# Optimization experiments

Hardware: AMD Instinct MI355X
Metric: run time of the kernel (lower is better)

## Reference

```python
import jax, jax.numpy as jnp
import numpy as np

B, N_IN, O, IN_L, OUT_L = 256, 1152, 10, 8, 16
ITERS = 3
EPS = 1e-7

def squash(s, eps):
    # norm over the capsule-length axis (-2), keepdim, as in the torch code
    dot = jnp.sum(s * s, axis=-2, keepdims=True)
    return (dot / (1.0 + dot) / jnp.sqrt(dot + eps)) * s

def setup_inputs() -> dict:
    key = jax.random.key(0)
    k1, k2, k3 = jax.random.split(key, 3)
    x = jax.random.normal(k1, (B, N_IN, IN_L, 1), dtype=jnp.float32)
    weight = 0.05 * jax.random.normal(k2, (1, N_IN, O, IN_L, OUT_L), dtype=jnp.float32)
    bias = 0.05 * jax.random.normal(k3, (1, 1, O, OUT_L, 1), dtype=jnp.float32)
    return {"x": x, "weight": weight, "bias": bias}

def reference(x, weight, bias):
    # u_hat[b,n,o,k] = sum_i W[0,n,o,i,k] * x[b,n,i,0]  -> (B, N, O, K, 1)
    u_hat = jnp.einsum('noik,bni->bnok', weight[0], x[..., 0])[..., None]
    u_det = jax.lax.stop_gradient(u_hat)
    b_ij = jnp.zeros((x.shape[0], N_IN, O, 1, 1), dtype=x.dtype)
    v = None
    for r in range(ITERS):
        c = jax.nn.softmax(b_ij, axis=2)          # routing coefficients over out caps
        u = u_hat if r == ITERS - 1 else u_det    # detached except last iter
        s = jnp.sum(c * u, axis=1, keepdims=True) + bias  # (B,1,O,K,1)
        v = squash(s, EPS)
        if r != ITERS - 1:
            # agreement: sum over capsule-length axis 3 -> (B,N,O,1,1)
            b_ij = b_ij + jnp.sum(u_det * v, axis=3, keepdims=True)
    return v
```

## Files before the change

### kernel.cpp

```cpp
#include <hip/hip_runtime.h>
#include <hip/hip_bf16.h>

#define BB   256
#define NIN  1152
#define OO   10
#define IL   8
#define OL   16
#define ROW  (OO*OL)
#define EPSQ 1e-7f
#define NT   4
#define BT   32

typedef unsigned short ushx8 __attribute__((ext_vector_type(8)));

__device__ __forceinline__ float bf2f(unsigned short h) {
    unsigned u = ((unsigned)h) << 16;
    return __builtin_bit_cast(float, u);
}

__global__ __launch_bounds__(160) void caps_build(
    const float* __restrict__ x, const float* __restrict__ w,
    unsigned short* __restrict__ u)
{
    __shared__ float4 wl4[NT][321];
    __shared__ float4 xl4[BT * 8];
    const int t  = threadIdx.x;
    const int n0 = blockIdx.x * NT;
    const int b0 = blockIdx.y * BT;

    const float4* wg = reinterpret_cast<const float4*>(w) + (size_t)n0 * 320;
    #pragma unroll
    for (int jj = 0; jj < 8; ++jj) {
        const int j   = t + jj * 160;
        const int row = j / 320;
        const int lin = j - row * 320;
        const int o   = lin >> 5;
        const int rem = lin & 31;
        const int i   = rem >> 2;
        const int kh  = rem & 3;
        wl4[row][(o << 5) | ((i ^ (o & 1)) << 2) | kh] = wg[j];
    }
    const float4* xg = reinterpret_cast<const float4*>(x);
    {
        int j = t;
        xl4[j] = xg[((size_t)(b0 + (j >> 3)) * NIN + n0) * 2 + (j & 7)];
        j = t + 160;
        if (j < BT * 8)
            xl4[j] = xg[((size_t)(b0 + (j >> 3)) * NIN + n0) * 2 + (j & 7)];
    }
    __syncthreads();

    const int nl = t / 40;
    const int r  = t - nl * 40;
    const int hh = r / 20;
    const int s  = r - hh * 20;
    const int o  = s >> 1;
    const int k8 = s & 1;
    const int p  = o & 1;
    const float4* wbase = &wl4[nl][(o << 5) | (k8 << 1)];
    const float4* xbase = &xl4[(hh * 16) * 8 + nl * 2];
    unsigned short* ub = u + ((size_t)(b0 + hh * 16) * NIN + n0 + nl) * ROW
                           + o * OL + k8 * 8;
    const size_t ustride = (size_t)NIN * ROW;

    for (int bl = 0; bl < 16; bl += 4) {
        float xv[4][IL];
        #pragma unroll
        for (int bb = 0; bb < 4; ++bb) {
            const float4 x0 = xbase[(bl + bb) * 8];
            const float4 x1 = xbase[(bl + bb) * 8 + 1];
            xv[bb][0] = x0.x; xv[bb][1] = x0.y; xv[bb][2] = x0.z; xv[bb][3] = x0.w;
            xv[bb][4] = x1.x; xv[bb][5] = x1.y; xv[bb][6] = x1.z; xv[bb][7] = x1.w;
        }

        float acc[4][8];
        #pragma unroll
        for (int bb = 0; bb < 4; ++bb)
            #pragma unroll
            for (int j = 0; j < 8; ++j) acc[bb][j] = 0.f;

        #pragma unroll
        for (int i = 0; i < IL; ++i) {
            const float4 wlo = wbase[(i ^ p) << 2];
            const float4 whi = wbase[((i ^ p) << 2) | 1];
            const float wv[8] = {wlo.x, wlo.y, wlo.z, wlo.w, whi.x, whi.y, whi.z, whi.w};
            #pragma unroll
            for (int bb = 0; bb < 4; ++bb)
                #pragma unroll
                for (int j = 0; j < 8; ++j)
                    acc[bb][j] = fmaf(wv[j], xv[bb][i], acc[bb][j]);
        }

        #pragma unroll
        for (int bb = 0; bb < 4; ++bb) {
            union { ushx8 v; __hip_bfloat162 h[4]; } pk;
            #pragma unroll
            for (int j = 0; j < 4; ++j)
                pk.h[j] = __float22bfloat162_rn(make_float2(acc[bb][2*j], acc[bb][2*j+1]));
            *reinterpret_cast<ushx8*>(ub + (size_t)(bl + bb) * ustride) = pk.v;
        }
    }
}

__global__ __launch_bounds__(768) void caps_route3(
    const unsigned short* __restrict__ u, const float* __restrict__ bias,
    float* __restrict__ outv)
{
    __shared__ float lds[12][ROW];
    __shared__ float vbuf[ROW];
    const int t  = threadIdx.x;
    const int q  = t & 3;
    const int g  = t >> 2;
    const int wv = t >> 6;
    const int b  = blockIdx.x;
    const unsigned short* ub = u + (size_t)b * NIN * ROW;

    float bsv = 0.f;
    if (t < ROW) bsv = bias[t];
    float vprev = 0.f;

    #pragma unroll
    for (int iter = 0; iter < 3; ++iter) {
        float sp[5][8];
        #pragma unroll
        for (int j = 0; j < 5; ++j)
            #pragma unroll
            for (int e = 0; e < 8; ++e) sp[j][e] = 0.f;

        if (iter == 0) {
            for (int m = 0; m < 6; ++m) {
                const unsigned short* un = ub + (size_t)(g + m * 192) * ROW;
                #pragma unroll
                for (int j = 0; j < 5; ++j) {
                    const ushx8 raw = *reinterpret_cast<const ushx8*>(un + (q + 4 * j) * 8);
                    #pragma unroll
                    for (int e = 0; e < 8; ++e) sp[j][e] += bf2f(raw[e]);
                }
            }
        } else {
            float vs[5][8];
            #pragma unroll
            for (int j = 0; j < 5; ++j) {
                #pragma unroll
                for (int e = 0; e < 8; ++e) vs[j][e] = vbuf[(q + 4 * j) * 8 + e];
            }

            for (int m = 0; m < 6; ++m) {
                const unsigned short* un = ub + (size_t)(g + m * 192) * ROW;
                float uf[5][8];
                #pragma unroll
                for (int j = 0; j < 5; ++j) {
                    const ushx8 raw = *reinterpret_cast<const ushx8*>(un + (q + 4 * j) * 8);
                    #pragma unroll
                    for (int e = 0; e < 8; ++e) uf[j][e] = bf2f(raw[e]);
                }

                float d[5], dd[5];
                #pragma unroll
                for (int j = 0; j < 5; ++j) {
                    float acc = uf[j][0] * vs[j][0];
                    #pragma unroll
                    for (int e = 1; e < 8; ++e) acc = fmaf(uf[j][e], vs[j][e], acc);
                    acc += __shfl_xor(acc, 1, 4);
                    d[j] = acc;
                }
                #pragma unroll
                for (int j = 0; j < 5; ++j) dd[j] = __shfl_xor(d[j], 2, 4);

                float mx = fmaxf(d[0], dd[0]);
                #pragma unroll
                for (int j = 1; j < 5; ++j) mx = fmaxf(mx, fmaxf(d[j], dd[j]));
                float se = 0.f, e_[5];
                #pragma unroll
                for (int j = 0; j < 5; ++j) {
                    e_[j] = __expf(d[j] - mx);
                    se += e_[j] + __expf(dd[j] - mx);
                }
                const float r = 1.f / se;
                #pragma unroll
                for (int j = 0; j < 5; ++j) {
                    const float c = e_[j] * r;
                    #pragma unroll
                    for (int e = 0; e < 8; ++e)
                        sp[j][e] = fmaf(c, uf[j][e], sp[j][e]);
                }
            }
        }

        #pragma unroll
        for (int j = 0; j < 5; ++j)
            #pragma unroll
            for (int e = 0; e < 8; ++e) {
                #pragma unroll
                for (int msk = 4; msk <= 32; msk <<= 1)
                    sp[j][e] += __shfl_xor(sp[j][e], msk);
            }
        if ((t & 63) < 4) {
            #pragma unroll
            for (int j = 0; j < 5; ++j)
                #pragma unroll
                for (int e = 0; e < 8; ++e)
                    lds[wv][(q + 4 * j) * 8 + e] = sp[j][e];
        }
        __syncthreads();

        if (t < ROW) {
            float ssum = 0.f;
            #pragma unroll
            for (int wvi = 0; wvi < 12; ++wvi) ssum += lds[wvi][t];
            const float sv = (iter == 0 ? 0.1f : 1.0f) * ssum + bsv;

            float dq = sv * sv;
            dq += __shfl_xor(dq, 1, 16);
            dq += __shfl_xor(dq, 2, 16);
            dq += __shfl_xor(dq, 4, 16);
            dq += __shfl_xor(dq, 8, 16);
            const float f = dq / ((1.f + dq) * sqrtf(dq + EPSQ));
            const float v = f * sv;

            if (iter == 0) { vbuf[t] = v; vprev = v; }
            else if (iter == 1) { vbuf[t] = v + vprev; }
            else { outv[(size_t)b * ROW + t] = v; }
        }
        __syncthreads();
    }
}

extern "C" void kernel_launch(void* const* d_in, const int* in_sizes, int n_in,
                              void* d_out, int out_size, void* d_ws, size_t ws_size,
                              hipStream_t stream) {
    const float* x    = (const float*)d_in[0];
    const float* w    = (const float*)d_in[1];
    const float* bias = (const float*)d_in[2];
    float* out = (float*)d_out;

    unsigned short* u = (unsigned short*)d_ws;

    caps_build<<<dim3(NIN / NT, BB / BT), 160, 0, stream>>>(x, w, u);
    caps_route3<<<BB, 768, 0, stream>>>(u, bias, out);
}
```

Measured before the change: 78.74 us.

## Split routing into per-iteration passes over two N-halves with finish kernels

Replaces the single fused three-iteration routing kernel (one block per batch) with separate pass kernels per iteration, each launched on a 256x2 grid that splits the input capsules into two halves. Small finish kernels combine the partial sums and apply bias and squash. Per-iteration v vectors go through global workspace instead of LDS. This doubles block count to fill more CUs, at the cost of six extra launches and global round trips between iterations.

```diff
diff --git a/kernel.cpp b/kernel.cpp
--- a/kernel.cpp
+++ b/kernel.cpp
@@ -102,128 +102,134 @@
     }
 }
 
-__global__ __launch_bounds__(768) void caps_route3(
-    const unsigned short* __restrict__ u, const float* __restrict__ bias,
-    float* __restrict__ outv)
+template<int ITER>
+__global__ __launch_bounds__(768) void caps_pass(
+    const unsigned short* __restrict__ u, const float* __restrict__ vin,
+    float* __restrict__ partial)
 {
     __shared__ float lds[12][ROW];
-    __shared__ float vbuf[ROW];
     const int t  = threadIdx.x;
     const int q  = t & 3;
     const int g  = t >> 2;
     const int wv = t >> 6;
     const int b  = blockIdx.x;
-    const unsigned short* ub = u + (size_t)b * NIN * ROW;
-
-    float bsv = 0.f;
-    if (t < ROW) bsv = bias[t];
-    float vprev = 0.f;
-
+    const int sp0 = blockIdx.y;
+    const unsigned short* ub = u + ((size_t)b * NIN + (size_t)sp0 * 576) * ROW;
+
+    float sp[5][8];
     #pragma unroll
-    for (int iter = 0; iter < 3; ++iter) {
-        float sp[5][8];
+    for (int j = 0; j < 5; ++j)
+        #pragma unroll
+        for (int e = 0; e < 8; ++e) sp[j][e] = 0.f;
+
+    if (ITER == 0) {
+        for (int m = 0; m < 3; ++m) {
+            const unsigned short* un = ub + (size_t)(g + m * 192) * ROW;
+            #pragma unroll
+            for (int j = 0; j < 5; ++j) {
+                const ushx8 raw = *reinterpret_cast<const ushx8*>(un + (q + 4 * j) * 8);
+                #pragma unroll
+                for (int e = 0; e < 8; ++e) sp[j][e] += bf2f(raw[e]);
+            }
+        }
+    } else {
+        float vs[5][8];
+        #pragma unroll
+        for (int j = 0; j < 5; ++j) {
+            const float* vp = vin + (size_t)b * ROW + (q + 4 * j) * 8;
+            const float4 a  = *reinterpret_cast<const float4*>(vp);
+            const float4 c4 = *reinterpret_cast<const float4*>(vp + 4);
+            vs[j][0] = a.x;  vs[j][1] = a.y;  vs[j][2] = a.z;  vs[j][3] = a.w;
+            vs[j][4] = c4.x; vs[j][5] = c4.y; vs[j][6] = c4.z; vs[j][7] = c4.w;
+        }
+
+        for (int m = 0; m < 3; ++m) {
+            const unsigned short* un = ub + (size_t)(g + m * 192) * ROW;
+            float uf[5][8];
+            #pragma unroll
+            for (int j = 0; j < 5; ++j) {
+                const ushx8 raw = *reinterpret_cast<const ushx8*>(un + (q + 4 * j) * 8);
+                #pragma unroll
+                for (int e = 0; e < 8; ++e) uf[j][e] = bf2f(raw[e]);
+            }
+
+            float d[5], dd[5];
+            #pragma unroll
+            for (int j = 0; j < 5; ++j) {
+                float acc = uf[j][0] * vs[j][0];
+                #pragma unroll
+                for (int e = 1; e < 8; ++e) acc = fmaf(uf[j][e], vs[j][e], acc);
+                acc += __shfl_xor(acc, 1, 4);
+                d[j] = acc;
+            }
+            #pragma unroll
+            for (int j = 0; j < 5; ++j) dd[j] = __shfl_xor(d[j], 2, 4);
+
+            float mx = fmaxf(d[0], dd[0]);
+            #pragma unroll
+            for (int j = 1; j < 5; ++j) mx = fmaxf(mx, fmaxf(d[j], dd[j]));
+            float se = 0.f, e_[5];
+            #pragma unroll
+            for (int j = 0; j < 5; ++j) {
+                e_[j] = __expf(d[j] - mx);
+                se += e_[j] + __expf(dd[j] - mx);
+            }
+            const float rr = 1.f / se;
+            #pragma unroll
+            for (int j = 0; j < 5; ++j) {
+                const float c = e_[j] * rr;
+                #pragma unroll
+                for (int e = 0; e < 8; ++e)
+                    sp[j][e] = fmaf(c, uf[j][e], sp[j][e]);
+            }
+        }
+    }
+
+    #pragma unroll
+    for (int j = 0; j < 5; ++j)
+        #pragma unroll
+        for (int e = 0; e < 8; ++e) {
+            #pragma unroll
+            for (int msk = 4; msk <= 32; msk <<= 1)
+                sp[j][e] += __shfl_xor(sp[j][e], msk);
+        }
+    if ((t & 63) < 4) {
         #pragma unroll
         for (int j = 0; j < 5; ++j)
             #pragma unroll
-            for (int e = 0; e < 8; ++e) sp[j][e] = 0.f;
-
-        if (iter == 0) {
-            for (int m = 0; m < 6; ++m) {
-                const unsigned short* un = ub + (size_t)(g + m * 192) * ROW;
-                #pragma unroll
-                for (int j = 0; j < 5; ++j) {
-                    const ushx8 raw = *reinterpret_cast<const ushx8*>(un + (q + 4 * j) * 8);
-                    #pragma unroll
-                    for (int e = 0; e < 8; ++e) sp[j][e] += bf2f(raw[e]);
-                }
-            }
-        } else {
-            float vs[5][8];
-            #pragma unroll
-            for (int j = 0; j < 5; ++j) {
-                #pragma unroll
-                for (int e = 0; e < 8; ++e) vs[j][e] = vbuf[(q + 4 * j) * 8 + e];
-            }
-
-            for (int m = 0; m < 6; ++m) {
-                const unsigned short* un = ub + (size_t)(g + m * 192) * ROW;
-                float uf[5][8];
-                #pragma unroll
-                for (int j = 0; j < 5; ++j) {
-                    const ushx8 raw = *reinterpret_cast<const ushx8*>(un + (q + 4 * j) * 8);
-                    #pragma unroll
-                    for (int e = 0; e < 8; ++e) uf[j][e] = bf2f(raw[e]);
-                }
-
-                float d[5], dd[5];
-                #pragma unroll
-                for (int j = 0; j < 5; ++j) {
-                    float acc = uf[j][0] * vs[j][0];
-                    #pragma unroll
-                    for (int e = 1; e < 8; ++e) acc = fmaf(uf[j][e], vs[j][e], acc);
-                    acc += __shfl_xor(acc, 1, 4);
-                    d[j] = acc;
-                }
-                #pragma unroll
-                for (int j = 0; j < 5; ++j) dd[j] = __shfl_xor(d[j], 2, 4);
-
-                float mx = fmaxf(d[0], dd[0]);
-                #pragma unroll
-                for (int j = 1; j < 5; ++j) mx = fmaxf(mx, fmaxf(d[j], dd[j]));
-                float se = 0.f, e_[5];
-                #pragma unroll
-                for (int j = 0; j < 5; ++j) {
-                    e_[j] = __expf(d[j] - mx);
-                    se += e_[j] + __expf(dd[j] - mx);
-                }
-                const float r = 1.f / se;
-                #pragma unroll
-                for (int j = 0; j < 5; ++j) {
-                    const float c = e_[j] * r;
-                    #pragma unroll
-                    for (int e = 0; e < 8; ++e)
-                        sp[j][e] = fmaf(c, uf[j][e], sp[j][e]);
-                }
-            }
-        }
-
-        #pragma unroll
-        for (int j = 0; j < 5; ++j)
-            #pragma unroll
-            for (int e = 0; e < 8; ++e) {
-                #pragma unroll
-                for (int msk = 4; msk <= 32; msk <<= 1)
-                    sp[j][e] += __shfl_xor(sp[j][e], msk);
-            }
-        if ((t & 63) < 4) {
-            #pragma unroll
-            for (int j = 0; j < 5; ++j)
-                #pragma unroll
-                for (int e = 0; e < 8; ++e)
-                    lds[wv][(q + 4 * j) * 8 + e] = sp[j][e];
-        }
-        __syncthreads();
-
-        if (t < ROW) {
-            float ssum = 0.f;
-            #pragma unroll
-            for (int wvi = 0; wvi < 12; ++wvi) ssum += lds[wvi][t];
-            const float sv = (iter == 0 ? 0.1f : 1.0f) * ssum + bsv;
-
-            float dq = sv * sv;
-            dq += __shfl_xor(dq, 1, 16);
-            dq += __shfl_xor(dq, 2, 16);
-            dq += __shfl_xor(dq, 4, 16);
-            dq += __shfl_xor(dq, 8, 16);
-            const float f = dq / ((1.f + dq) * sqrtf(dq + EPSQ));
-            const float v = f * sv;
-
-            if (iter == 0) { vbuf[t] = v; vprev = v; }
-            else if (iter == 1) { vbuf[t] = v + vprev; }
-            else { outv[(size_t)b * ROW + t] = v; }
-        }
-        __syncthreads();
-    }
+            for (int e = 0; e < 8; ++e)
+                lds[wv][(q + 4 * j) * 8 + e] = sp[j][e];
+    }
+    __syncthreads();
+
+    if (t < ROW) {
+        float ssum = 0.f;
+        #pragma unroll
+        for (int wvi = 0; wvi < 12; ++wvi) ssum += lds[wvi][t];
+        partial[((size_t)sp0 * BB + b) * ROW + t] = ssum;
+    }
+}
+
+__global__ __launch_bounds__(192) void caps_finish(
+    const float* __restrict__ partial, const float* __restrict__ bias,
+    const float* __restrict__ prevAdd, float* __restrict__ outv, float scale)
+{
+    const int t = threadIdx.x;
+    if (t >= ROW) return;
+    const int b = blockIdx.x;
+
+    const float s = scale * (partial[(size_t)b * ROW + t]
+                           + partial[((size_t)BB + b) * ROW + t]) + bias[t];
+
+    float d = s * s;
+    d += __shfl_xor(d, 1, 16);
+    d += __shfl_xor(d, 2, 16);
+    d += __shfl_xor(d, 4, 16);
+    d += __shfl_xor(d, 8, 16);
+    const float f = d / ((1.f + d) * sqrtf(d + EPSQ));
+    float v = f * s;
+    if (prevAdd) v += prevAdd[(size_t)b * ROW + t];
+    outv[(size_t)b * ROW + t] = v;
 }
 
 extern "C" void kernel_launch(void* const* d_in, const int* in_sizes, int n_in,
@@ -235,7 +241,17 @@
     float* out = (float*)d_out;
 
     unsigned short* u = (unsigned short*)d_ws;
+    float* partial = (float*)((char*)d_ws + (size_t)BB * NIN * ROW * 2);
+    float* v0  = partial + (size_t)2 * BB * ROW;
+    float* vsb = v0 + (size_t)BB * ROW;
+
+    const dim3 pg(BB, 2);
 
     caps_build<<<dim3(NIN / NT, BB / BT), 160, 0, stream>>>(x, w, u);
-    caps_route3<<<BB, 768, 0, stream>>>(u, bias, out);
-}
+    caps_pass<0><<<pg, 768, 0, stream>>>(u, nullptr, partial);
+    caps_finish<<<BB, 192, 0, stream>>>(partial, bias, nullptr, v0, 0.1f);
+    caps_pass<1><<<pg, 768, 0, stream>>>(u, v0, partial);
+    caps_finish<<<BB, 192, 0, stream>>>(partial, bias, v0, vsb, 1.0f);
+    caps_pass<2><<<pg, 768, 0, stream>>>(u, vsb, partial);
+    caps_finish<<<BB, 192, 0, stream>>>(partial, bias, nullptr, out, 1.0f);
+}
```

Result: slower. 100.3 us (+27.4%).

## Compute first routing iteration directly from x and W, skipping a pass over u

Applied to the files above, without the earlier changes.

The first routing iteration has uniform coefficients, so its weighted sum equals one tenth of the plain sum of u_hat over input capsules. That sum is now computed by a new fp32 GEMM-style kernel that writes per-chunk partial sums, followed by a small squash kernel. The routing kernel then runs only the two remaining iterations, saving one full read of the large bf16 u tensor. In exchange it adds two launches, extra reads of x and W, and a partial-sum buffer in workspace.

```diff
diff --git a/kernel.cpp b/kernel.cpp
--- a/kernel.cpp
+++ b/kernel.cpp
@@ -10,6 +10,7 @@
 #define EPSQ 1e-7f
 #define NT   4
 #define BT   32
+#define GNC  72
 
 typedef unsigned short ushx8 __attribute__((ext_vector_type(8)));
 
@@ -102,9 +103,91 @@
     }
 }
 
-__global__ __launch_bounds__(768) void caps_route3(
+__global__ __launch_bounds__(320) void caps_gemm0(
+    const float* __restrict__ x, const float* __restrict__ w,
+    float* __restrict__ psum)
+{
+    const int t   = threadIdx.x;
+    const int bq  = t / 20;
+    const int oct = t - bq * 20;
+    const int o   = oct >> 1;
+    const int k8  = oct & 1;
+    const int b1  = blockIdx.x * 32 + bq;
+    const int b2  = b1 + 16;
+    const int nc  = blockIdx.y;
+    const int n0  = nc * 16;
+
+    const float* wq  = w + (size_t)n0 * 1280 + o * 128 + k8 * 8;
+    const float* xq1 = x + ((size_t)b1 * NIN + n0) * 8;
+    const float* xq2 = x + ((size_t)b2 * NIN + n0) * 8;
+
+    float a0[8], a1[8];
+    #pragma unroll
+    for (int j = 0; j < 8; ++j) { a0[j] = 0.f; a1[j] = 0.f; }
+
+    for (int nn = 0; nn < 16; ++nn) {
+        const float4 xa0 = *reinterpret_cast<const float4*>(xq1 + nn * 8);
+        const float4 xa1 = *reinterpret_cast<const float4*>(xq1 + nn * 8 + 4);
+        const float4 xb0 = *reinterpret_cast<const float4*>(xq2 + nn * 8);
+        const float4 xb1 = *reinterpret_cast<const float4*>(xq2 + nn * 8 + 4);
+        const float xv0[IL] = {xa0.x, xa0.y, xa0.z, xa0.w, xa1.x, xa1.y, xa1.z, xa1.w};
+        const float xv1[IL] = {xb0.x, xb0.y, xb0.z, xb0.w, xb1.x, xb1.y, xb1.z, xb1.w};
+
+        const float* wn = wq + (size_t)nn * 1280;
+        #pragma unroll
+        for (int i = 0; i < IL; ++i) {
+            const float4 wlo = *reinterpret_cast<const float4*>(wn + i * 16);
+            const float4 whi = *reinterpret_cast<const float4*>(wn + i * 16 + 4);
+            a0[0] = fmaf(wlo.x, xv0[i], a0[0]);  a1[0] = fmaf(wlo.x, xv1[i], a1[0]);
+            a0[1] = fmaf(wlo.y, xv0[i], a0[1]);  a1[1] = fmaf(wlo.y, xv1[i], a1[1]);
+            a0[2] = fmaf(wlo.z, xv0[i], a0[2]);  a1[2] = fmaf(wlo.z, xv1[i], a1[2]);
+            a0[3] = fmaf(wlo.w, xv0[i], a0[3]);  a1[3] = fmaf(wlo.w, xv1[i], a1[3]);
+            a0[4] = fmaf(whi.x, xv0[i], a0[4]);  a1[4] = fmaf(whi.x, xv1[i], a1[4]);
+            a0[5] = fmaf(whi.y, xv0[i], a0[5]);  a1[5] = fmaf(whi.y, xv1[i], a1[5]);
+            a0[6] = fmaf(whi.z, xv0[i], a0[6]);  a1[6] = fmaf(whi.z, xv1[i], a1[6]);
+            a0[7] = fmaf(whi.w, xv0[i], a0[7]);  a1[7] = fmaf(whi.w, xv1[i], a1[7]);
+        }
+    }
+
+    float* p1 = psum + ((size_t)nc * BB + b1) * ROW + oct * 8;
+    float* p2 = psum + ((size_t)nc * BB + b2) * ROW + oct * 8;
+    *reinterpret_cast<float4*>(p1)     = make_float4(a0[0], a0[1], a0[2], a0[3]);
+    *reinterpret_cast<float4*>(p1 + 4) = make_float4(a0[4], a0[5], a0[6], a0[7]);
+    *reinterpret_cast<float4*>(p2)     = make_float4(a1[0], a1[1], a1[2], a1[3]);
+    *reinterpret_cast<float4*>(p2 + 4) = make_float4(a1[4], a1[5], a1[6], a1[7]);
+}
+
+__global__ __launch_bounds__(192) void caps_squash0(
+    const float* __restrict__ psum, const float* __restrict__ bias,
+    float* __restrict__ v0)
+{
+    const int t = threadIdx.x;
+    if (t >= ROW) return;
+    const int b = blockIdx.x;
+
+    float s0 = 0.f, s1 = 0.f, s2 = 0.f, s3 = 0.f;
+    const float* pt = psum + (size_t)b * ROW + t;
+    #pragma unroll
+    for (int ch = 0; ch < GNC; ch += 4) {
+        s0 += pt[(size_t)(ch + 0) * BB * ROW];
+        s1 += pt[(size_t)(ch + 1) * BB * ROW];
+        s2 += pt[(size_t)(ch + 2) * BB * ROW];
+        s3 += pt[(size_t)(ch + 3) * BB * ROW];
+    }
+    const float s = 0.1f * ((s0 + s1) + (s2 + s3)) + bias[t];
+
+    float d = s * s;
+    d += __shfl_xor(d, 1, 16);
+    d += __shfl_xor(d, 2, 16);
+    d += __shfl_xor(d, 4, 16);
+    d += __shfl_xor(d, 8, 16);
+    const float f = d / ((1.f + d) * sqrtf(d + EPSQ));
+    v0[(size_t)b * ROW + t] = f * s;
+}
+
+__global__ __launch_bounds__(768) void caps_route2(
     const unsigned short* __restrict__ u, const float* __restrict__ bias,
-    float* __restrict__ outv)
+    const float* __restrict__ v0g, float* __restrict__ outv)
 {
     __shared__ float lds[12][ROW];
     __shared__ float vbuf[ROW];
@@ -116,74 +199,68 @@
     const unsigned short* ub = u + (size_t)b * NIN * ROW;
 
     float bsv = 0.f;
-    if (t < ROW) bsv = bias[t];
     float vprev = 0.f;
+    if (t < ROW) {
+        bsv = bias[t];
+        const float v = v0g[(size_t)b * ROW + t];
+        vbuf[t] = v;
+        vprev = v;
+    }
+    __syncthreads();
 
     #pragma unroll
-    for (int iter = 0; iter < 3; ++iter) {
+    for (int iter = 1; iter < 3; ++iter) {
         float sp[5][8];
         #pragma unroll
         for (int j = 0; j < 5; ++j)
             #pragma unroll
             for (int e = 0; e < 8; ++e) sp[j][e] = 0.f;
 
-        if (iter == 0) {
-            for (int m = 0; m < 6; ++m) {
-                const unsigned short* un = ub + (size_t)(g + m * 192) * ROW;
-                #pragma unroll
-                for (int j = 0; j < 5; ++j) {
-                    const ushx8 raw = *reinterpret_cast<const ushx8*>(un + (q + 4 * j) * 8);
-                    #pragma unroll
-                    for (int e = 0; e < 8; ++e) sp[j][e] += bf2f(raw[e]);
-                }
-            }
-        } else {
-            float vs[5][8];
+        float vs[5][8];
+        #pragma unroll
+        for (int j = 0; j < 5; ++j) {
+            #pragma unroll
+            for (int e = 0; e < 8; ++e) vs[j][e] = vbuf[(q + 4 * j) * 8 + e];
+        }
+
+        for (int m = 0; m < 6; ++m) {
+            const unsigned short* un = ub + (size_t)(g + m * 192) * ROW;
+            float uf[5][8];
             #pragma unroll
             for (int j = 0; j < 5; ++j) {
-                #pragma unroll
-                for (int e = 0; e < 8; ++e) vs[j][e] = vbuf[(q + 4 * j) * 8 + e];
-            }
-
-            for (int m = 0; m < 6; ++m) {
-                const unsigned short* un = ub + (size_t)(g + m * 192) * ROW;
-                float uf[5][8];
-                #pragma unroll
-                for (int j = 0; j < 5; ++j) {
-                    const ushx8 raw = *reinterpret_cast<const ushx8*>(un + (q + 4 * j) * 8);
-                    #pragma unroll
-                    for (int e = 0; e < 8; ++e) uf[j][e] = bf2f(raw[e]);
-                }
-
-                float d[5], dd[5];
-                #pragma unroll
-                for (int j = 0; j < 5; ++j) {
-                    float acc = uf[j][0] * vs[j][0];
-                    #pragma unroll
-                    for (int e = 1; e < 8; ++e) acc = fmaf(uf[j][e], vs[j][e], acc);
-                    acc += __shfl_xor(acc, 1, 4);
-                    d[j] = acc;
-                }
-                #pragma unroll
-                for (int j = 0; j < 5; ++j) dd[j] = __shfl_xor(d[j], 2, 4);
-
-                float mx = fmaxf(d[0], dd[0]);
-                #pragma unroll
-                for (int j = 1; j < 5; ++j) mx = fmaxf(mx, fmaxf(d[j], dd[j]));
-                float se = 0.f, e_[5];
-                #pragma unroll
-                for (int j = 0; j < 5; ++j) {
-                    e_[j] = __expf(d[j] - mx);
-                    se += e_[j] + __expf(dd[j] - mx);
-                }
-                const float r = 1.f / se;
-                #pragma unroll
-                for (int j = 0; j < 5; ++j) {
-                    const float c = e_[j] * r;
-                    #pragma unroll
-                    for (int e = 0; e < 8; ++e)
-                        sp[j][e] = fmaf(c, uf[j][e], sp[j][e]);
-                }
+                const ushx8 raw = *reinterpret_cast<const ushx8*>(un + (q + 4 * j) * 8);
+                #pragma unroll
+                for (int e = 0; e < 8; ++e) uf[j][e] = bf2f(raw[e]);
+            }
+
+            float d[5], dd[5];
+            #pragma unroll
+            for (int j = 0; j < 5; ++j) {
+                float acc = uf[j][0] * vs[j][0];
+                #pragma unroll
+                for (int e = 1; e < 8; ++e) acc = fmaf(uf[j][e], vs[j][e], acc);
+                acc += __shfl_xor(acc, 1, 4);
+                d[j] = acc;
+            }
+            #pragma unroll
+            for (int j = 0; j < 5; ++j) dd[j] = __shfl_xor(d[j], 2, 4);
+
+            float mx = fmaxf(d[0], dd[0]);
+            #pragma unroll
+            for (int j = 1; j < 5; ++j) mx = fmaxf(mx, fmaxf(d[j], dd[j]));
+            float se = 0.f, e_[5];
+            #pragma unroll
+            for (int j = 0; j < 5; ++j) {
+                e_[j] = __expf(d[j] - mx);
+                se += e_[j] + __expf(dd[j] - mx);
+            }
+            const float rr = 1.f / se;
+            #pragma unroll
+            for (int j = 0; j < 5; ++j) {
+                const float c = e_[j] * rr;
+                #pragma unroll
+                for (int e = 0; e < 8; ++e)
+                    sp[j][e] = fmaf(c, uf[j][e], sp[j][e]);
             }
         }
 
@@ -208,7 +285,7 @@
             float ssum = 0.f;
             #pragma unroll
             for (int wvi = 0; wvi < 12; ++wvi) ssum += lds[wvi][t];
-            const float sv = (iter == 0 ? 0.1f : 1.0f) * ssum + bsv;
+            const float sv = ssum + bsv;
 
             float dq = sv * sv;
             dq += __shfl_xor(dq, 1, 16);
@@ -218,9 +295,8 @@
             const float f = dq / ((1.f + dq) * sqrtf(dq + EPSQ));
             const float v = f * sv;
 
-            if (iter == 0) { vbuf[t] = v; vprev = v; }
-            else if (iter == 1) { vbuf[t] = v + vprev; }
-            else { outv[(size_t)b * ROW + t] = v; }
+            if (iter == 1) { vbuf[t] = v + vprev; }
+            else           { outv[(size_t)b * ROW + t] = v; }
         }
         __syncthreads();
     }
@@ -235,7 +311,11 @@
     float* out = (float*)d_out;
 
     unsigned short* u = (unsigned short*)d_ws;
+    float* psum = (float*)((char*)d_ws + (size_t)BB * NIN * ROW * 2);
+    float* v0   = psum + (size_t)GNC * BB * ROW;
 
     caps_build<<<dim3(NIN / NT, BB / BT), 160, 0, stream>>>(x, w, u);
-    caps_route3<<<BB, 768, 0, stream>>>(u, bias, out);
-}
+    caps_gemm0<<<dim3(BB / 32, GNC), 320, 0, stream>>>(x, w, psum);
+    caps_squash0<<<BB, 192, 0, stream>>>(psum, bias, v0);
+    caps_route2<<<BB, 768, 0, stream>>>(u, bias, v0, out);
+}
```

Measured after the change: 130.0 us. 1.65x slower.

## Compute first routing iteration sum via MFMA GEMM over x and W instead of u

Applied to the files above, without the earlier changes.

The first routing iteration uses uniform coefficients, so its sum over input capsules equals a contraction of x with W. A new split-K MFMA bf16 kernel computes these partial sums directly from x and W, and the routing kernel reduces the partials and skips its first full pass over the large bf16 u tensor. This saves one read of u per batch at the cost of an extra launch, partial-sum traffic, and bf16 rounding of x and W in the GEMM.

```diff
diff --git a/kernel.cpp b/kernel.cpp
--- a/kernel.cpp
+++ b/kernel.cpp
@@ -10,12 +10,20 @@
 #define EPSQ 1e-7f
 #define NT   4
 #define BT   32
+#define KSP  8
 
 typedef unsigned short ushx8 __attribute__((ext_vector_type(8)));
+typedef short s16x8 __attribute__((ext_vector_type(8)));
+typedef float f32x4 __attribute__((ext_vector_type(4)));
 
 __device__ __forceinline__ float bf2f(unsigned short h) {
     unsigned u = ((unsigned)h) << 16;
     return __builtin_bit_cast(float, u);
+}
+__device__ __forceinline__ unsigned short f2bf(float f) {
+    unsigned u = __builtin_bit_cast(unsigned, f);
+    u += 0x7FFFu + ((u >> 16) & 1u);
+    return (unsigned short)(u >> 16);
 }
 
 __global__ __launch_bounds__(160) void caps_build(
@@ -102,9 +110,50 @@
     }
 }
 
-__global__ __launch_bounds__(768) void caps_route3(
+__global__ __launch_bounds__(256) void caps_gemm0(
+    const float* __restrict__ x, const float* __restrict__ w,
+    float* __restrict__ psum)
+{
+    const int t   = threadIdx.x;
+    const int l   = t & 63;
+    const int wv  = t >> 6;
+    const int idx = blockIdx.x * 4 + wv;
+    const int bt  = idx / 10;
+    const int ct  = idx - bt * 10;
+    const int ks  = blockIdx.y;
+    const int l15 = l & 15, lg = l >> 4;
+    const int b   = bt * 16 + l15;
+
+    f32x4 acc = (f32x4){0.f, 0.f, 0.f, 0.f};
+
+    #pragma unroll 4
+    for (int kstep = 0; kstep < 36; ++kstep) {
+        const int n = ks * 144 + kstep * 4 + lg;
+
+        const float* xpn = x + ((size_t)b * NIN + n) * 8;
+        const float4 xa = *reinterpret_cast<const float4*>(xpn);
+        const float4 xc = *reinterpret_cast<const float4*>(xpn + 4);
+        union { s16x8 v; unsigned short h[8]; } A;
+        A.h[0] = f2bf(xa.x); A.h[1] = f2bf(xa.y); A.h[2] = f2bf(xa.z); A.h[3] = f2bf(xa.w);
+        A.h[4] = f2bf(xc.x); A.h[5] = f2bf(xc.y); A.h[6] = f2bf(xc.z); A.h[7] = f2bf(xc.w);
+
+        const float* wb = w + (((size_t)n * OO + ct) * IL) * OL + l15;
+        union { s16x8 v; unsigned short h[8]; } B;
+        #pragma unroll
+        for (int i = 0; i < IL; ++i) B.h[i] = f2bf(wb[i * OL]);
+
+        acc = __builtin_amdgcn_mfma_f32_16x16x32_bf16(A.v, B.v, acc, 0, 0, 0);
+    }
+
+    float* pb = psum + ((size_t)ks * BB + bt * 16 + lg * 4) * ROW + ct * OL + l15;
+    #pragma unroll
+    for (int r = 0; r < 4; ++r)
+        pb[(size_t)r * ROW] = acc[r];
+}
+
+__global__ __launch_bounds__(768) void caps_route2(
     const unsigned short* __restrict__ u, const float* __restrict__ bias,
-    float* __restrict__ outv)
+    const float* __restrict__ psum, float* __restrict__ outv)
 {
     __shared__ float lds[12][ROW];
     __shared__ float vbuf[ROW];
@@ -116,74 +165,80 @@
     const unsigned short* ub = u + (size_t)b * NIN * ROW;
 
     float bsv = 0.f;
-    if (t < ROW) bsv = bias[t];
     float vprev = 0.f;
+    if (t < ROW) {
+        bsv = bias[t];
+        const float* pt = psum + (size_t)b * ROW + t;
+        float s0 = pt[0];
+        #pragma unroll
+        for (int ks = 1; ks < KSP; ++ks) s0 += pt[(size_t)ks * BB * ROW];
+        const float s = 0.1f * s0 + bsv;
+
+        float d = s * s;
+        d += __shfl_xor(d, 1, 16);
+        d += __shfl_xor(d, 2, 16);
+        d += __shfl_xor(d, 4, 16);
+        d += __shfl_xor(d, 8, 16);
+        const float f = d / ((1.f + d) * sqrtf(d + EPSQ));
+        const float v = f * s;
+        vbuf[t] = v;
+        vprev = v;
+    }
+    __syncthreads();
 
     #pragma unroll
-    for (int iter = 0; iter < 3; ++iter) {
+    for (int iter = 1; iter < 3; ++iter) {
         float sp[5][8];
         #pragma unroll
         for (int j = 0; j < 5; ++j)
             #pragma unroll
             for (int e = 0; e < 8; ++e) sp[j][e] = 0.f;
 
-        if (iter == 0) {
-            for (int m = 0; m < 6; ++m) {
-                const unsigned short* un = ub + (size_t)(g + m * 192) * ROW;
-                #pragma unroll
-                for (int j = 0; j < 5; ++j) {
-                    const ushx8 raw = *reinterpret_cast<const ushx8*>(un + (q + 4 * j) * 8);
-                    #pragma unroll
-                    for (int e = 0; e < 8; ++e) sp[j][e] += bf2f(raw[e]);
-                }
-            }
-        } else {
-            float vs[5][8];
-            #pragma unroll
-            for (int j = 0; j < 5; ++j) {
-                #pragma unroll
-                for (int e = 0; e < 8; ++e) vs[j][e] = vbuf[(q + 4 * j) * 8 + e];
-            }
-
-            for (int m = 0; m < 6; ++m) {
-                const unsigned short* un = ub + (size_t)(g + m * 192) * ROW;
-                float uf[5][8];
-                #pragma unroll
-                for (int j = 0; j < 5; ++j) {
-                    const ushx8 raw = *reinterpret_cast<const ushx8*>(un + (q + 4 * j) * 8);
-                    #pragma unroll
-                    for (int e = 0; e < 8; ++e) uf[j][e] = bf2f(raw[e]);
-                }
-
-                float d[5], dd[5];
-                #pragma unroll
-                for (int j = 0; j < 5; ++j) {
-                    float acc = uf[j][0] * vs[j][0];
-                    #pragma unroll
-                    for (int e = 1; e < 8; ++e) acc = fmaf(uf[j][e], vs[j][e], acc);
-                    acc += __shfl_xor(acc, 1, 4);
-                    d[j] = acc;
-                }
-                #pragma unroll
-                for (int j = 0; j < 5; ++j) dd[j] = __shfl_xor(d[j], 2, 4);
-
-                float mx = fmaxf(d[0], dd[0]);
-                #pragma unroll
-                for (int j = 1; j < 5; ++j) mx = fmaxf(mx, fmaxf(d[j], dd[j]));
-                float se = 0.f, e_[5];
-                #pragma unroll
-                for (int j = 0; j < 5; ++j) {
-                    e_[j] = __expf(d[j] - mx);
-                    se += e_[j] + __expf(dd[j] - mx);
-                }
-                const float r = 1.f / se;
-                #pragma unroll
-                for (int j = 0; j < 5; ++j) {
-                    const float c = e_[j] * r;
-                    #pragma unroll
-                    for (int e = 0; e < 8; ++e)
-                        sp[j][e] = fmaf(c, uf[j][e], sp[j][e]);
-                }
+        float vs[5][8];
+        #pragma unroll
+        for (int j = 0; j < 5; ++j) {
+            #pragma unroll
+            for (int e = 0; e < 8; ++e) vs[j][e] = vbuf[(q + 4 * j) * 8 + e];
+        }
+
+        for (int m = 0; m < 6; ++m) {
+            const unsigned short* un = ub + (size_t)(g + m * 192) * ROW;
+            float uf[5][8];
+            #pragma unroll
+            for (int j = 0; j < 5; ++j) {
+                const ushx8 raw = *reinterpret_cast<const ushx8*>(un + (q + 4 * j) * 8);
+                #pragma unroll
+                for (int e = 0; e < 8; ++e) uf[j][e] = bf2f(raw[e]);
+            }
+
+            float d[5], dd[5];
+            #pragma unroll
+            for (int j = 0; j < 5; ++j) {
+                float acc = uf[j][0] * vs[j][0];
+                #pragma unroll
+                for (int e = 1; e < 8; ++e) acc = fmaf(uf[j][e], vs[j][e], acc);
+                acc += __shfl_xor(acc, 1, 4);
+                d[j] = acc;
+            }
+            #pragma unroll
+            for (int j = 0; j < 5; ++j) dd[j] = __shfl_xor(d[j], 2, 4);
+
+            float mx = fmaxf(d[0], dd[0]);
+            #pragma unroll
+            for (int j = 1; j < 5; ++j) mx = fmaxf(mx, fmaxf(d[j], dd[j]));
+            float se = 0.f, e_[5];
+            #pragma unroll
+            for (int j = 0; j < 5; ++j) {
+                e_[j] = __expf(d[j] - mx);
+                se += e_[j] + __expf(dd[j] - mx);
+            }
+            const float rr = 1.f / se;
+            #pragma unroll
+            for (int j = 0; j < 5; ++j) {
+                const float c = e_[j] * rr;
+                #pragma unroll
+                for (int e = 0; e < 8; ++e)
+                    sp[j][e] = fmaf(c, uf[j][e], sp[j][e]);
             }
         }
 
@@ -208,7 +263,7 @@
             float ssum = 0.f;
             #pragma unroll
             for (int wvi = 0; wvi < 12; ++wvi) ssum += lds[wvi][t];
-            const float sv = (iter == 0 ? 0.1f : 1.0f) * ssum + bsv;
+            const float sv = ssum + bsv;
 
             float dq = sv * sv;
             dq += __shfl_xor(dq, 1, 16);
@@ -218,9 +273,8 @@
             const float f = dq / ((1.f + dq) * sqrtf(dq + EPSQ));
             const float v = f * sv;
 
-            if (iter == 0) { vbuf[t] = v; vprev = v; }
-            else if (iter == 1) { vbuf[t] = v + vprev; }
-            else { outv[(size_t)b * ROW + t] = v; }
+            if (iter == 1) { vbuf[t] = v + vprev; }
+            else           { outv[(size_t)b * ROW + t] = v; }
         }
         __syncthreads();
     }
@@ -235,7 +289,9 @@
     float* out = (float*)d_out;
 
     unsigned short* u = (unsigned short*)d_ws;
+    float* psum = (float*)((char*)d_ws + (size_t)BB * NIN * ROW * 2);
 
     caps_build<<<dim3(NIN / NT, BB / BT), 160, 0, stream>>>(x, w, u);
-    caps_route3<<<BB, 768, 0, stream>>>(u, bias, out);
-}
+    caps_gemm0<<<dim3(40, KSP), 256, 0, stream>>>(x, w, psum);
+    caps_route2<<<BB, 768, 0, stream>>>(u, bias, psum, out);
+}
```

Result: slower. 87.42 us (+11.0%).
